# Performance work log

Hardware: AMD Instinct MI355X
Metric: run time of the kernel (lower is better)

The kernel has to match this reference:

```python
import jax, jax.numpy as jnp
import numpy as np

N = 100000          # nodes
E = 3200000         # edges (avg degree 32)
F_IN = 128
HID = [128, 256, 128, 64, 32]
EPS = 1e-5


def setup_inputs() -> dict:
    key = jax.random.key(0)
    ks = jax.random.split(key, 64)
    inp = {}
    inp["x"] = jax.random.normal(ks[0], (N, F_IN), dtype=jnp.float32)
    inp["edge_index"] = jax.random.randint(ks[1], (2, E), 0, N, dtype=jnp.int64)
    dims = [F_IN] + HID
    k = 2
    for i in range(len(HID)):
        fan_in = dims[i]
        inp[f"W{i}"] = jax.random.normal(ks[k], (dims[i], dims[i + 1]), dtype=jnp.float32) / np.sqrt(fan_in); k += 1
        inp[f"b{i}"] = jnp.zeros((dims[i + 1],), dtype=jnp.float32)
        inp[f"g{i}"] = jnp.ones((dims[i + 1],), dtype=jnp.float32)
        inp[f"be{i}"] = jnp.zeros((dims[i + 1],), dtype=jnp.float32)
    inp["fc_w"] = jax.random.normal(ks[k], (HID[-1], 1), dtype=jnp.float32) / np.sqrt(HID[-1])
    inp["fc_b"] = jnp.zeros((1,), dtype=jnp.float32)
    return inp


def _gcn_forward(x, edge_index, Ws, bs, gs, bes, fc_w, fc_b):
    src, dst = edge_index[0], edge_index[1]
    # symmetric-normalized adjacency with self-loops (PyG GCNConv default,
    # edge_weight=None -> all-ones). deg = in-degree + 1 (self-loop).
    deg = jax.ops.segment_sum(jnp.ones((E,), x.dtype), dst, num_segments=N) + 1.0
    dis = jax.lax.rsqrt(deg)                 # deg^{-1/2}
    di = 1.0 / deg                           # self-loop norm deg^{-1}
    norm = (dis[src] * dis[dst])[:, None]    # [E,1]
    for W, b, g, be in zip(Ws, bs, gs, bes):
        h = x @ W                                                        # [N,d']
        x = jax.ops.segment_sum(norm * h[src], dst, num_segments=N)
        x = x + di[:, None] * h + b                                      # conv out
        mu = jnp.mean(x, axis=0)
        var = jnp.mean(jnp.square(x - mu), axis=0)
        x = (x - mu) * jax.lax.rsqrt(var + EPS) * g + be                 # BatchNorm1d
        x = jax.nn.relu(x)                                               # dropout = eval identity
    edge_emb = x[src] * x[dst]                                           # [E, 32]
    return jax.nn.sigmoid(edge_emb @ fc_w + fc_b)                        # [E, 1]


def reference(x, edge_index, W0, b0, g0, be0, W1, b1, g1, be1, W2, b2, g2, be2,
              W3, b3, g3, be3, W4, b4, g4, be4, fc_w, fc_b):
    Ws = [W0, W1, W2, W3, W4]
    bs = [b0, b1, b2, b3, b4]
    gs = [g0, g1, g2, g3, g4]
    bes = [be0, be1, be2, be3, be4]
    return _gcn_forward(x, edge_index, Ws, bs, gs, bes, fc_w, fc_b)
```

## Files before the change

kernel.cpp:

```cpp
#include <hip/hip_runtime.h>
#include <hip/hip_fp16.h>
#include <cstddef>

#define NN 100000
#define EE 3200000
#define EPSB 1e-5f
#define NB 391
#define BCAP 10240
#define BNBLK 512

typedef _Float16 half8 __attribute__((ext_vector_type(8)));
typedef float floatx4 __attribute__((ext_vector_type(4)));


__global__ __launch_bounds__(256) void k_bscat(const int* __restrict__ src,
                                               const int* __restrict__ dst,
                                               int* __restrict__ bcur,
                                               unsigned* __restrict__ barr) {
    __shared__ int hist[NB];
    __shared__ int base[NB];
    int tid = threadIdx.x;
    for (int b = tid; b < NB; b += 256) hist[b] = 0;
    __syncthreads();
    int e0 = blockIdx.x * 4096;
    int d[16], s[16];
    #pragma unroll
    for (int j = 0; j < 16; j++) {
        int e = e0 + j * 256 + tid;
        if (e < EE) {
            d[j] = dst[e];
            s[j] = src[e];
            atomicAdd(&hist[d[j] >> 8], 1);
        } else d[j] = -1;
    }
    __syncthreads();
    for (int b = tid; b < NB; b += 256) {
        int c = hist[b];
        base[b] = (c > 0) ? atomicAdd(&bcur[b], c) : 0;
        hist[b] = 0;
    }
    __syncthreads();
    #pragma unroll
    for (int j = 0; j < 16; j++) {
        if (d[j] >= 0) {
            int b = d[j] >> 8;
            int r = atomicAdd(&hist[b], 1);
            barr[(size_t)b * BCAP + base[b] + r] =
                (unsigned)s[j] | ((unsigned)(d[j] & 255) << 17);
        }
    }
}

__global__ __launch_bounds__(1024) void k_bdeg(const int* __restrict__ bcur,
                                               const unsigned* __restrict__ barr,
                                               int* __restrict__ degcnt,
                                               float* __restrict__ dis) {
    __shared__ int h[256];
    int b = blockIdx.x;
    if (threadIdx.x < 256) h[threadIdx.x] = 0;
    __syncthreads();
    int cnt = bcur[b];
    const unsigned* p = barr + (size_t)b * BCAP;
    for (int t = threadIdx.x; t < cnt; t += 1024)
        atomicAdd(&h[(p[t] >> 17) & 255], 1);
    __syncthreads();
    if (threadIdx.x < 256) {
        int node = (b << 8) + threadIdx.x;
        if (node < NN) {
            int dg = h[threadIdx.x];
            degcnt[node] = dg;
            dis[node] = rsqrtf((float)dg + 1.0f);
        }
    }
}

__global__ __launch_bounds__(1024) void k_place(const int* __restrict__ bcur,
                                                const unsigned* __restrict__ barr,
                                                const int* __restrict__ rowptr,
                                                int* __restrict__ col) {
    __shared__ int cur[256];
    int b = blockIdx.x;
    if (threadIdx.x < 256) {
        int node = (b << 8) + threadIdx.x;
        cur[threadIdx.x] = (node < NN) ? rowptr[node] : 0;
    }
    __syncthreads();
    int cnt = bcur[b];
    const unsigned* p = barr + (size_t)b * BCAP;
    for (int t = threadIdx.x; t < cnt; t += 1024) {
        unsigned e = p[t];
        int pos = atomicAdd(&cur[(e >> 17) & 255], 1);
        col[pos] = (int)(e & 0x1FFFFu);
    }
}

__global__ void k_scan_block(const int* __restrict__ in, int* __restrict__ out,
                             int* __restrict__ blksum, int n) {
    __shared__ int s[1024];
    int i = blockIdx.x * 1024 + threadIdx.x;
    int v = (i < n) ? in[i] : 0;
    s[threadIdx.x] = v;
    __syncthreads();
    for (int off = 1; off < 1024; off <<= 1) {
        int t = (threadIdx.x >= off) ? s[threadIdx.x - off] : 0;
        __syncthreads();
        s[threadIdx.x] += t;
        __syncthreads();
    }
    if (i < n) out[i] = s[threadIdx.x] - v;
    if (threadIdx.x == 1023) blksum[blockIdx.x] = s[1023];
}

__global__ void k_scan_top(int* __restrict__ blksum, int nb) {
    if (threadIdx.x == 0) {
        int acc = 0;
        for (int b = 0; b < nb; b++) { int v = blksum[b]; blksum[b] = acc; acc += v; }
    }
}

__global__ void k_scan_add(int* __restrict__ out, const int* __restrict__ blksum, int n) {
    int i = blockIdx.x * 1024 + threadIdx.x;
    if (i < n) out[i] += blksum[blockIdx.x];
}


__global__ void k_f2h(const float4* __restrict__ in, uint2* __restrict__ out, int n4) {
    int t = blockIdx.x * blockDim.x + threadIdx.x;
    if (t >= n4) return;
    float4 v = in[t];
    union { __half2 h; unsigned u; } a, b;
    a.h = __floats2half2_rn(v.x, v.y);
    b.h = __floats2half2_rn(v.z, v.w);
    out[t] = make_uint2(a.u, b.u);
}

__global__ void k_wpack_all(const float* __restrict__ W0, const float* __restrict__ W1,
                            const float* __restrict__ W2, const float* __restrict__ W3,
                            const float* __restrict__ W4, __half* __restrict__ Wp) {
    const int offs[6] = {0, 16384, 49152, 81920, 90112, 92160};
    const int Ks[5] = {128, 128, 256, 128, 64};
    const int Ns[5] = {128, 256, 128, 64, 32};
    const float* Ws[5] = {W0, W1, W2, W3, W4};
    int t = blockIdx.x * blockDim.x + threadIdx.x;
    if (t >= 92160) return;
    int l = 0;
    while (t >= offs[l + 1]) l++;
    int local = t - offs[l];
    int N = Ns[l], K = Ks[l];
    int k = local / N, n = local - k * N;
    Wp[(size_t)offs[l] + (size_t)n * K + k] = __float2half(Ws[l][local]);
}


template<int NT, bool OUT16>
__global__ __launch_bounds__(256) void k_mgemm(const __half* __restrict__ A,
                                               const __half* __restrict__ Wp,
                                               void* __restrict__ Cv,
                                               int M, int K, int N,
                                               const float* __restrict__ dis,
                                               const float* __restrict__ bias) {
    constexpr int TN = NT * 16;
    __shared__ __half Ash[128][40];
    __shared__ __half Bsh[TN][40];
    int tid  = threadIdx.x;
    int wave = tid >> 6;
    int lane = tid & 63;
    int quad = lane >> 4;
    int l16  = lane & 15;
    int bm = blockIdx.x * 128;
    int bn = blockIdx.y * TN;

    floatx4 acc[2][NT];
    #pragma unroll
    for (int mt = 0; mt < 2; mt++)
        #pragma unroll
        for (int nt = 0; nt < NT; nt++)
            acc[mt][nt] = (floatx4){0.f, 0.f, 0.f, 0.f};

    for (int k0 = 0; k0 < K; k0 += 32) {
        #pragma unroll
        for (int it = 0; it < 2; it++) {
            int u = tid + it * 256;
            int row = u >> 2, seg = u & 3;
            int grow = bm + row;
            uint4 v = make_uint4(0, 0, 0, 0);
            if (grow < M) v = *(const uint4*)&A[(size_t)grow * K + k0 + seg * 8];
            *(uint4*)&Ash[row][seg * 8] = v;
        }
        if (tid < TN * 4) {
            int n = tid >> 2, seg = tid & 3;
            uint4 v = *(const uint4*)&Wp[(size_t)(bn + n) * K + k0 + seg * 8];
            *(uint4*)&Bsh[n][seg * 8] = v;
        }
        __syncthreads();
        half8 a[2], b[NT];
        #pragma unroll
        for (int mt = 0; mt < 2; mt++)
            a[mt] = *(const half8*)&Ash[wave * 32 + mt * 16 + l16][quad * 8];
        #pragma unroll
        for (int nt = 0; nt < NT; nt++)
            b[nt] = *(const half8*)&Bsh[nt * 16 + l16][quad * 8];
        #pragma unroll
        for (int mt = 0; mt < 2; mt++)
            #pragma unroll
            for (int nt = 0; nt < NT; nt++)
                acc[mt][nt] = __builtin_amdgcn_mfma_f32_16x16x32_f16(
                    a[mt], b[nt], acc[mt][nt], 0, 0, 0);
        __syncthreads();
    }

    #pragma unroll
    for (int mt = 0; mt < 2; mt++) {
        #pragma unroll
        for (int r = 0; r < 4; r++) {
            int grow = bm + wave * 32 + mt * 16 + quad * 4 + r;
            if (grow >= M) continue;
            if (OUT16) {
                float ds = dis[grow];
                __half* C = (__half*)Cv;
                #pragma unroll
                for (int nt = 0; nt < NT; nt++) {
                    int gcol = bn + nt * 16 + l16;
                    C[(size_t)grow * N + gcol] = __float2half(ds * acc[mt][nt][r]);
                }
            } else {
                float* C = (float*)Cv;
                #pragma unroll
                for (int nt = 0; nt < NT; nt++) {
                    int gcol = bn + nt * 16 + l16;
                    C[(size_t)grow * N + gcol] = acc[mt][nt][r] + bias[gcol];
                }
            }
        }
    }
}

__global__ void k_scale16(const uint4* __restrict__ X, const float* __restrict__ dis,
                          uint4* __restrict__ out) {
    int t = blockIdx.x * blockDim.x + threadIdx.x;
    if (t >= NN * 16) return;
    int row = t >> 4;
    float ds = dis[row];
    uint4 v = X[t];
    const __half2* hp = (const __half2*)&v;
    uint4 o;
    __half2* op = (__half2*)&o;
    #pragma unroll
    for (int k = 0; k < 4; k++) {
        float2 f = __half22float2(hp[k]);
        op[k] = __floats2half2_rn(ds * f.x, ds * f.y);
    }
    out[t] = o;
}


__device__ __forceinline__ void acc_row(float* acc, const uint4& r) {
    const __half2* hp = (const __half2*)&r;
    #pragma unroll
    for (int k = 0; k < 4; k++) {
        float2 f2 = __half22float2(hp[k]);
        acc[2 * k]     += f2.x;
        acc[2 * k + 1] += f2.y;
    }
}

template<int TPN, bool OUT16>
__global__ __launch_bounds__(256) void k_agg_h(const uint4* __restrict__ Hs,
                                               void* __restrict__ outv,
                                               const int* __restrict__ rowptr,
                                               const int* __restrict__ degcnt,
                                               const int* __restrict__ colv,
                                               const float* __restrict__ dis,
                                               const float* __restrict__ bias) {
    constexpr int G = 256 / TPN;
    int g    = threadIdx.x / TPN;
    int lane = threadIdx.x % TPN;
    int i = blockIdx.x * G + g;
    if (i >= NN) return;
    int beg = rowptr[i];
    int cnt = degcnt[i];
    const uint4* base = Hs + lane;
    float acc[8] = {};
    int e = 0;
    for (; e + 8 <= cnt; e += 8) {
        int c[8];
        #pragma unroll
        for (int j = 0; j < 8; j++) c[j] = colv[beg + e + j];
        uint4 r[8];
        #pragma unroll
        for (int j = 0; j < 8; j++) r[j] = base[(size_t)c[j] * TPN];
        #pragma unroll
        for (int j = 0; j < 8; j++) acc_row(acc, r[j]);
    }
    for (; e < cnt; e++) {
        uint4 r = base[(size_t)colv[beg + e] * TPN];
        acc_row(acc, r);
    }
    uint4 rs = base[(size_t)i * TPN];
    acc_row(acc, rs);
    float ds = dis[i];
    float o[8];
    #pragma unroll
    for (int k = 0; k < 8; k++) o[k] = ds * acc[k];
    if (OUT16) {
        uint4 ov;
        __half2* op = (__half2*)&ov;
        #pragma unroll
        for (int k = 0; k < 4; k++) op[k] = __floats2half2_rn(o[2 * k], o[2 * k + 1]);
        ((uint4*)outv)[(size_t)i * TPN + lane] = ov;
    } else {
        float4 b0 = ((const float4*)bias)[lane * 2];
        float4 b1 = ((const float4*)bias)[lane * 2 + 1];
        o[0] += b0.x; o[1] += b0.y; o[2] += b0.z; o[3] += b0.w;
        o[4] += b1.x; o[5] += b1.y; o[6] += b1.z; o[7] += b1.w;
        float4* out = (float4*)outv;
        size_t ob = (size_t)i * (2 * TPN) + lane * 2;
        out[ob]     = make_float4(o[0], o[1], o[2], o[3]);
        out[ob + 1] = make_float4(o[4], o[5], o[6], o[7]);
    }
}


template<int D>
__global__ __launch_bounds__(256) void k_bnpart(const float4* __restrict__ X4,
                                                float* __restrict__ partial) {
    constexpr int Q   = D / 4;
    constexpr int RPI = 256 / Q;
    int tq = threadIdx.x % Q;
    int rg = threadIdx.x / Q;
    int chunk = (NN + BNBLK - 1) / BNBLK;
    int r0 = blockIdx.x * chunk;
    int r1 = r0 + chunk; if (r1 > NN) r1 = NN;
    float4 s  = {0.f, 0.f, 0.f, 0.f};
    float4 s2 = {0.f, 0.f, 0.f, 0.f};
    for (int r = r0 + rg; r < r1; r += RPI) {
        float4 v = X4[(size_t)r * Q + tq];
        s.x += v.x; s.y += v.y; s.z += v.z; s.w += v.w;
        s2.x += v.x * v.x; s2.y += v.y * v.y; s2.z += v.z * v.z; s2.w += v.w * v.w;
    }
    __shared__ float4 ls[256], ls2[256];
    ls[threadIdx.x] = s; ls2[threadIdx.x] = s2;
    __syncthreads();
    if (threadIdx.x < Q) {
        float4 a = ls[threadIdx.x], b = ls2[threadIdx.x];
        #pragma unroll
        for (int g = 1; g < RPI; g++) {
            float4 u = ls[g * Q + threadIdx.x], w = ls2[g * Q + threadIdx.x];
            a.x += u.x; a.y += u.y; a.z += u.z; a.w += u.w;
            b.x += w.x; b.y += w.y; b.z += w.z; b.w += w.w;
        }
        *(float4*)&partial[(size_t)blockIdx.x * 2 * D + threadIdx.x * 4]     = a;
        *(float4*)&partial[(size_t)blockIdx.x * 2 * D + D + threadIdx.x * 4] = b;
    }
}

template<int D>
__global__ void k_bnfin2(const float* __restrict__ partial, const float* __restrict__ g,
                         const float* __restrict__ be, float* __restrict__ AB) {
    int f = threadIdx.x;
    if (f < D) {
        float sum = 0.f, sq = 0.f;
        for (int b = 0; b < BNBLK; b++) {
            sum += partial[(size_t)b * 2 * D + f];
            sq  += partial[(size_t)b * 2 * D + D + f];
        }
        float mu  = sum / (float)NN;
        float var = sq / (float)NN - mu * mu;
        var = fmaxf(var, 0.f);
        float inv = rsqrtf(var + EPSB);
        float a = g[f] * inv;
        AB[f]     = a;
        AB[D + f] = be[f] - mu * a;
    }
}

__global__ void k_norm16(const float4* __restrict__ X, const float* __restrict__ AB,
                         uint2* __restrict__ Y, int d, int total4) {
    int t = blockIdx.x * blockDim.x + threadIdx.x;
    if (t >= total4) return;
    int f0 = (t * 4) & (d - 1);
    float4 v = X[t];
    float a0 = AB[f0],     a1 = AB[f0 + 1], a2 = AB[f0 + 2], a3 = AB[f0 + 3];
    float c0 = AB[d + f0], c1 = AB[d + f0 + 1], c2 = AB[d + f0 + 2], c3 = AB[d + f0 + 3];
    float o0 = fmaxf(v.x * a0 + c0, 0.f);
    float o1 = fmaxf(v.y * a1 + c1, 0.f);
    float o2 = fmaxf(v.z * a2 + c2, 0.f);
    float o3 = fmaxf(v.w * a3 + c3, 0.f);
    union { __half2 h; unsigned u; } p, q;
    p.h = __floats2half2_rn(o0, o1);
    q.h = __floats2half2_rn(o2, o3);
    Y[t] = make_uint2(p.u, q.u);
}


__global__ __launch_bounds__(256) void k_edge16(const uint4* __restrict__ X,
                                                const int* __restrict__ src,
                                                const int* __restrict__ dst,
                                                const float* __restrict__ fcw,
                                                const float* __restrict__ fcb,
                                                float* __restrict__ out) {
    int lane = threadIdx.x & 3;
    size_t t = (size_t)blockIdx.x * 256 + threadIdx.x;
    int eid = (int)(t >> 2);
    if (eid >= EE) return;
    int s = src[eid], d = dst[eid];
    uint4 av = X[(size_t)s * 4 + lane];
    uint4 bv = X[(size_t)d * 4 + lane];
    const __half2* ap = (const __half2*)&av;
    const __half2* bp2 = (const __half2*)&bv;
    float v = 0.f;
    #pragma unroll
    for (int k = 0; k < 4; k++) {
        float2 fa = __half22float2(ap[k]);
        float2 fb = __half22float2(bp2[k]);
        float w0 = fcw[lane * 8 + 2 * k];
        float w1 = fcw[lane * 8 + 2 * k + 1];
        v += fa.x * fb.x * w0 + fa.y * fb.y * w1;
    }
    v += __shfl_xor(v, 1, 4);
    v += __shfl_xor(v, 2, 4);
    if (lane == 0) out[eid] = 1.f / (1.f + expf(-(v + fcb[0])));
}


extern "C" void kernel_launch(void* const* d_in, const int* in_sizes, int n_in,
                              void* d_out, int out_size, void* d_ws, size_t ws_size,
                              hipStream_t stream) {
    const float* x0 = (const float*)d_in[0];
    const int* ei   = (const int*)d_in[1];
    const int* srcv = ei;
    const int* dstv = ei + EE;
    const float *W[5], *bp[5], *gp[5], *bep[5];
    int idx = 2;
    for (int l = 0; l < 5; l++) {
        W[l]   = (const float*)d_in[idx++];
        bp[l]  = (const float*)d_in[idx++];
        gp[l]  = (const float*)d_in[idx++];
        bep[l] = (const float*)d_in[idx++];
    }
    const float* fcw = (const float*)d_in[22];
    const float* fcb = (const float*)d_in[23];

    char* ws = (char*)d_ws;
    size_t off = 0;
    auto alloc = [&](size_t bytes) -> void* {
        void* p = ws + off;
        off = (off + bytes + 255) & ~(size_t)255;
        return p;
    };
    float*    bufA    = (float*)   alloc((size_t)NN * 256 * 4);
    __half*   act16   = (__half*)  alloc((size_t)NN * 256 * 2);
    __half*   x16     = (__half*)  alloc((size_t)NN * 128 * 2);
    __half*   Hh      = (__half*)  alloc((size_t)NN * 128 * 2);
    unsigned* barr    = (unsigned*)alloc((size_t)NB * BCAP * 4);
    int*      colv    = (int*)     alloc((size_t)EE * 4);
    int*      rowptr  = (int*)     alloc((size_t)NN * 4);
    int*      degcnt  = (int*)     alloc((size_t)NN * 4);
    float*    dis     = (float*)   alloc((size_t)NN * 4);
    int*      bcur    = (int*)     alloc((size_t)NB * 4);
    int*      scnblk  = (int*)     alloc(4096);
    float*    bnpart  = (float*)   alloc((size_t)BNBLK * 512 * 4);
    float*    bnAB    = (float*)   alloc(512 * 4);
    __half*   Wp      = (__half*)  alloc((size_t)92160 * 2);
    const int woff[5] = {0, 16384, 49152, 81920, 90112};

    hipMemsetAsync(bcur, 0, (size_t)NB * 4, stream);
    k_bscat<<<(EE + 4095) / 4096, 256, 0, stream>>>(srcv, dstv, bcur, barr);
    k_bdeg<<<NB, 1024, 0, stream>>>(bcur, barr, degcnt, dis);
    int nScanBlk = (NN + 1023) / 1024;
    k_scan_block<<<nScanBlk, 1024, 0, stream>>>(degcnt, rowptr, scnblk, NN);
    k_scan_top<<<1, 64, 0, stream>>>(scnblk, nScanBlk);
    k_scan_add<<<nScanBlk, 1024, 0, stream>>>(rowptr, scnblk, NN);
    k_place<<<NB, 1024, 0, stream>>>(bcur, barr, rowptr, colv);

    k_f2h<<<(NN * 128 / 4 + 255) / 256, 256, 0, stream>>>(
        (const float4*)x0, (uint2*)x16, NN * 128 / 4);
    k_wpack_all<<<(92160 + 255) / 256, 256, 0, stream>>>(W[0], W[1], W[2], W[3], W[4], Wp);

    int gx = (NN + 127) / 128;

    {
        dim3 grid(gx, 128 / 64);
        k_mgemm<4, true><<<grid, 256, 0, stream>>>(x16, Wp + woff[0], Hh, NN, 128, 128, dis, nullptr);
        k_agg_h<16, false><<<(NN + 15) / 16, 256, 0, stream>>>(
            (const uint4*)Hh, bufA, rowptr, degcnt, colv, dis, bp[0]);
        k_bnpart<128><<<BNBLK, 256, 0, stream>>>((const float4*)bufA, bnpart);
        k_bnfin2<128><<<1, 256, 0, stream>>>(bnpart, gp[0], bep[0], bnAB);
        int total4 = NN * 128 / 4;
        k_norm16<<<(total4 + 255) / 256, 256, 0, stream>>>(
            (const float4*)bufA, bnAB, (uint2*)act16, 128, total4);
    }
    {
        k_scale16<<<(NN * 16 + 255) / 256, 256, 0, stream>>>(
            (const uint4*)act16, dis, (uint4*)Hh);
        k_agg_h<16, true><<<(NN + 15) / 16, 256, 0, stream>>>(
            (const uint4*)Hh, act16, rowptr, degcnt, colv, dis, nullptr);
        dim3 grid(gx, 256 / 64);
        k_mgemm<4, false><<<grid, 256, 0, stream>>>(act16, Wp + woff[1], bufA, NN, 128, 256, nullptr, bp[1]);
        k_bnpart<256><<<BNBLK, 256, 0, stream>>>((const float4*)bufA, bnpart);
        k_bnfin2<256><<<1, 256, 0, stream>>>(bnpart, gp[1], bep[1], bnAB);
        int total4 = NN * 256 / 4;
        k_norm16<<<(total4 + 255) / 256, 256, 0, stream>>>(
            (const float4*)bufA, bnAB, (uint2*)act16, 256, total4);
    }
    {
        dim3 grid(gx, 128 / 64);
        k_mgemm<4, true><<<grid, 256, 0, stream>>>(act16, Wp + woff[2], Hh, NN, 256, 128, dis, nullptr);
        k_agg_h<16, false><<<(NN + 15) / 16, 256, 0, stream>>>(
            (const uint4*)Hh, bufA, rowptr, degcnt, colv, dis, bp[2]);
        k_bnpart<128><<<BNBLK, 256, 0, stream>>>((const float4*)bufA, bnpart);
        k_bnfin2<128><<<1, 256, 0, stream>>>(bnpart, gp[2], bep[2], bnAB);
        int total4 = NN * 128 / 4;
        k_norm16<<<(total4 + 255) / 256, 256, 0, stream>>>(
            (const float4*)bufA, bnAB, (uint2*)act16, 128, total4);
    }
    {
        dim3 grid(gx, 64 / 64);
        k_mgemm<4, true><<<grid, 256, 0, stream>>>(act16, Wp + woff[3], Hh, NN, 128, 64, dis, nullptr);
        k_agg_h<8, false><<<(NN + 31) / 32, 256, 0, stream>>>(
            (const uint4*)Hh, bufA, rowptr, degcnt, colv, dis, bp[3]);
        k_bnpart<64><<<BNBLK, 256, 0, stream>>>((const float4*)bufA, bnpart);
        k_bnfin2<64><<<1, 256, 0, stream>>>(bnpart, gp[3], bep[3], bnAB);
        int total4 = NN * 64 / 4;
        k_norm16<<<(total4 + 255) / 256, 256, 0, stream>>>(
            (const float4*)bufA, bnAB, (uint2*)act16, 64, total4);
    }
    {
        dim3 grid(gx, 1);
        k_mgemm<2, true><<<grid, 256, 0, stream>>>(act16, Wp + woff[4], Hh, NN, 64, 32, dis, nullptr);
        k_agg_h<4, false><<<(NN + 63) / 64, 256, 0, stream>>>(
            (const uint4*)Hh, bufA, rowptr, degcnt, colv, dis, bp[4]);
        k_bnpart<32><<<BNBLK, 256, 0, stream>>>((const float4*)bufA, bnpart);
        k_bnfin2<32><<<1, 256, 0, stream>>>(bnpart, gp[4], bep[4], bnAB);
        int total4 = NN * 32 / 4;
        k_norm16<<<(total4 + 255) / 256, 256, 0, stream>>>(
            (const float4*)bufA, bnAB, (uint2*)act16, 32, total4);
    }

    size_t edgeThreads = (size_t)EE * 4;
    k_edge16<<<(unsigned)((edgeThreads + 255) / 256), 256, 0, stream>>>(
        (const uint4*)act16, srcv, dstv, fcw, fcb, (float*)d_out);
}
```

Before: 1.015 ms.

## Fuse BatchNorm-ReLU into GEMM A-load and dis scaling; parallelize BN finalize

Removes the separate BN-normalize kernels for layers 0-3. Layer 0's BN+ReLU is folded into the dis-scaling pass before aggregation. Layers 1-3 apply BN+ReLU on the fly while the next GEMM loads its fp32 A tile into LDS. The BN finalize kernel now uses 1024 threads with a shared-memory reduction instead of a serial loop over 512 partials. This saves a full write and read of the activations per layer, but the GEMM now reads fp32 A (twice the bytes) and recomputes the normalization for every N-tile block.

```diff
diff --git a/kernel.cpp b/kernel.cpp
--- a/kernel.cpp
+++ b/kernel.cpp
@@ -152,13 +152,14 @@
 }
 
 
-template<int NT, bool OUT16>
-__global__ __launch_bounds__(256) void k_mgemm(const __half* __restrict__ A,
+template<int NT, bool OUT16, bool ABN>
+__global__ __launch_bounds__(256) void k_mgemm(const void* __restrict__ Av,
                                                const __half* __restrict__ Wp,
                                                void* __restrict__ Cv,
                                                int M, int K, int N,
                                                const float* __restrict__ dis,
-                                               const float* __restrict__ bias) {
+                                               const float* __restrict__ bias,
+                                               const float* __restrict__ AB) {
     constexpr int TN = NT * 16;
     __shared__ __half Ash[128][40];
     __shared__ __half Bsh[TN][40];
@@ -183,9 +184,39 @@
             int u = tid + it * 256;
             int row = u >> 2, seg = u & 3;
             int grow = bm + row;
-            uint4 v = make_uint4(0, 0, 0, 0);
-            if (grow < M) v = *(const uint4*)&A[(size_t)grow * K + k0 + seg * 8];
-            *(uint4*)&Ash[row][seg * 8] = v;
+            if (ABN) {
+                const float* Af = (const float*)Av;
+                int f0 = k0 + seg * 8;
+                uint4 o = make_uint4(0, 0, 0, 0);
+                if (grow < M) {
+                    float4 x0 = *(const float4*)&Af[(size_t)grow * K + f0];
+                    float4 x1 = *(const float4*)&Af[(size_t)grow * K + f0 + 4];
+                    float4 a0 = *(const float4*)&AB[f0];
+                    float4 a1 = *(const float4*)&AB[f0 + 4];
+                    float4 c0 = *(const float4*)&AB[K + f0];
+                    float4 c1 = *(const float4*)&AB[K + f0 + 4];
+                    float h0 = fmaxf(x0.x * a0.x + c0.x, 0.f);
+                    float h1 = fmaxf(x0.y * a0.y + c0.y, 0.f);
+                    float h2 = fmaxf(x0.z * a0.z + c0.z, 0.f);
+                    float h3 = fmaxf(x0.w * a0.w + c0.w, 0.f);
+                    float h4 = fmaxf(x1.x * a1.x + c1.x, 0.f);
+                    float h5 = fmaxf(x1.y * a1.y + c1.y, 0.f);
+                    float h6 = fmaxf(x1.z * a1.z + c1.z, 0.f);
+                    float h7 = fmaxf(x1.w * a1.w + c1.w, 0.f);
+                    union { __half2 h; unsigned u; } p0, p1, p2, p3;
+                    p0.h = __floats2half2_rn(h0, h1);
+                    p1.h = __floats2half2_rn(h2, h3);
+                    p2.h = __floats2half2_rn(h4, h5);
+                    p3.h = __floats2half2_rn(h6, h7);
+                    o = make_uint4(p0.u, p1.u, p2.u, p3.u);
+                }
+                *(uint4*)&Ash[row][seg * 8] = o;
+            } else {
+                const __half* A = (const __half*)Av;
+                uint4 v = make_uint4(0, 0, 0, 0);
+                if (grow < M) v = *(const uint4*)&A[(size_t)grow * K + k0 + seg * 8];
+                *(uint4*)&Ash[row][seg * 8] = v;
+            }
         }
         if (tid < TN * 4) {
             int n = tid >> 2, seg = tid & 3;
@@ -235,22 +266,33 @@
     }
 }
 
-__global__ void k_scale16(const uint4* __restrict__ X, const float* __restrict__ dis,
-                          uint4* __restrict__ out) {
+__global__ void k_nscale(const float* __restrict__ X, const float* __restrict__ AB,
+                         const float* __restrict__ dis, uint4* __restrict__ out) {
     int t = blockIdx.x * blockDim.x + threadIdx.x;
     if (t >= NN * 16) return;
     int row = t >> 4;
+    int f0 = (t & 15) * 8;
     float ds = dis[row];
-    uint4 v = X[t];
-    const __half2* hp = (const __half2*)&v;
-    uint4 o;
-    __half2* op = (__half2*)&o;
-    #pragma unroll
-    for (int k = 0; k < 4; k++) {
-        float2 f = __half22float2(hp[k]);
-        op[k] = __floats2half2_rn(ds * f.x, ds * f.y);
-    }
-    out[t] = o;
+    float4 x0 = *(const float4*)&X[(size_t)row * 128 + f0];
+    float4 x1 = *(const float4*)&X[(size_t)row * 128 + f0 + 4];
+    float4 a0 = *(const float4*)&AB[f0];
+    float4 a1 = *(const float4*)&AB[f0 + 4];
+    float4 c0 = *(const float4*)&AB[128 + f0];
+    float4 c1 = *(const float4*)&AB[128 + f0 + 4];
+    float h0 = ds * fmaxf(x0.x * a0.x + c0.x, 0.f);
+    float h1 = ds * fmaxf(x0.y * a0.y + c0.y, 0.f);
+    float h2 = ds * fmaxf(x0.z * a0.z + c0.z, 0.f);
+    float h3 = ds * fmaxf(x0.w * a0.w + c0.w, 0.f);
+    float h4 = ds * fmaxf(x1.x * a1.x + c1.x, 0.f);
+    float h5 = ds * fmaxf(x1.y * a1.y + c1.y, 0.f);
+    float h6 = ds * fmaxf(x1.z * a1.z + c1.z, 0.f);
+    float h7 = ds * fmaxf(x1.w * a1.w + c1.w, 0.f);
+    union { __half2 h; unsigned u; } p0, p1, p2, p3;
+    p0.h = __floats2half2_rn(h0, h1);
+    p1.h = __floats2half2_rn(h2, h3);
+    p2.h = __floats2half2_rn(h4, h5);
+    p3.h = __floats2half2_rn(h6, h7);
+    out[t] = make_uint4(p0.u, p1.u, p2.u, p3.u);
 }
 
 
@@ -355,22 +397,34 @@
 }
 
 template<int D>
-__global__ void k_bnfin2(const float* __restrict__ partial, const float* __restrict__ g,
-                         const float* __restrict__ be, float* __restrict__ AB) {
-    int f = threadIdx.x;
-    if (f < D) {
-        float sum = 0.f, sq = 0.f;
-        for (int b = 0; b < BNBLK; b++) {
-            sum += partial[(size_t)b * 2 * D + f];
-            sq  += partial[(size_t)b * 2 * D + D + f];
-        }
-        float mu  = sum / (float)NN;
-        float var = sq / (float)NN - mu * mu;
+__global__ __launch_bounds__(1024) void k_bnfin2(const float* __restrict__ partial,
+                                                 const float* __restrict__ g,
+                                                 const float* __restrict__ be,
+                                                 float* __restrict__ AB) {
+    constexpr int G = 1024 / D;
+    int f  = threadIdx.x % D;
+    int gr = threadIdx.x / D;
+    float sum = 0.f, sq = 0.f;
+    for (int b = gr; b < BNBLK; b += G) {
+        sum += partial[(size_t)b * 2 * D + f];
+        sq  += partial[(size_t)b * 2 * D + D + f];
+    }
+    __shared__ float ls[1024], ls2[1024];
+    ls[threadIdx.x] = sum; ls2[threadIdx.x] = sq;
+    __syncthreads();
+    if (threadIdx.x < D) {
+        float a = ls[threadIdx.x], b = ls2[threadIdx.x];
+        for (int k = 1; k < G; k++) {
+            a += ls[k * D + threadIdx.x];
+            b += ls2[k * D + threadIdx.x];
+        }
+        float mu  = a / (float)NN;
+        float var = b / (float)NN - mu * mu;
         var = fmaxf(var, 0.f);
         float inv = rsqrtf(var + EPSB);
-        float a = g[f] * inv;
-        AB[f]     = a;
-        AB[D + f] = be[f] - mu * a;
+        float sc = g[threadIdx.x] * inv;
+        AB[threadIdx.x]     = sc;
+        AB[D + threadIdx.x] = be[threadIdx.x] - mu * sc;
     }
 }
 
@@ -481,57 +535,44 @@
 
     {
         dim3 grid(gx, 128 / 64);
-        k_mgemm<4, true><<<grid, 256, 0, stream>>>(x16, Wp + woff[0], Hh, NN, 128, 128, dis, nullptr);
+        k_mgemm<4, true, false><<<grid, 256, 0, stream>>>(x16, Wp + woff[0], Hh, NN, 128, 128, dis, nullptr, nullptr);
         k_agg_h<16, false><<<(NN + 15) / 16, 256, 0, stream>>>(
             (const uint4*)Hh, bufA, rowptr, degcnt, colv, dis, bp[0]);
         k_bnpart<128><<<BNBLK, 256, 0, stream>>>((const float4*)bufA, bnpart);
-        k_bnfin2<128><<<1, 256, 0, stream>>>(bnpart, gp[0], bep[0], bnAB);
-        int total4 = NN * 128 / 4;
-        k_norm16<<<(total4 + 255) / 256, 256, 0, stream>>>(
-            (const float4*)bufA, bnAB, (uint2*)act16, 128, total4);
+        k_bnfin2<128><<<1, 1024, 0, stream>>>(bnpart, gp[0], bep[0], bnAB);
+        k_nscale<<<(NN * 16 + 255) / 256, 256, 0, stream>>>(bufA, bnAB, dis, (uint4*)Hh);
     }
     {
-        k_scale16<<<(NN * 16 + 255) / 256, 256, 0, stream>>>(
-            (const uint4*)act16, dis, (uint4*)Hh);
         k_agg_h<16, true><<<(NN + 15) / 16, 256, 0, stream>>>(
             (const uint4*)Hh, act16, rowptr, degcnt, colv, dis, nullptr);
         dim3 grid(gx, 256 / 64);
-        k_mgemm<4, false><<<grid, 256, 0, stream>>>(act16, Wp + woff[1], bufA, NN, 128, 256, nullptr, bp[1]);
+        k_mgemm<4, false, false><<<grid, 256, 0, stream>>>(act16, Wp + woff[1], bufA, NN, 128, 256, nullptr, bp[1], nullptr);
         k_bnpart<256><<<BNBLK, 256, 0, stream>>>((const float4*)bufA, bnpart);
-        k_bnfin2<256><<<1, 256, 0, stream>>>(bnpart, gp[1], bep[1], bnAB);
-        int total4 = NN * 256 / 4;
-        k_norm16<<<(total4 + 255) / 256, 256, 0, stream>>>(
-            (const float4*)bufA, bnAB, (uint2*)act16, 256, total4);
+        k_bnfin2<256><<<1, 1024, 0, stream>>>(bnpart, gp[1], bep[1], bnAB);
     }
     {
         dim3 grid(gx, 128 / 64);
-        k_mgemm<4, true><<<grid, 256, 0, stream>>>(act16, Wp + woff[2], Hh, NN, 256, 128, dis, nullptr);
+        k_mgemm<4, true, true><<<grid, 256, 0, stream>>>(bufA, Wp + woff[2], Hh, NN, 256, 128, dis, nullptr, bnAB);
         k_agg_h<16, false><<<(NN + 15) / 16, 256, 0, stream>>>(
             (const uint4*)Hh, bufA, rowptr, degcnt, colv, dis, bp[2]);
         k_bnpart<128><<<BNBLK, 256, 0, stream>>>((const float4*)bufA, bnpart);
-        k_bnfin2<128><<<1, 256, 0, stream>>>(bnpart, gp[2], bep[2], bnAB);
-        int total4 = NN * 128 / 4;
-        k_norm16<<<(total4 + 255) / 256, 256, 0, stream>>>(
-            (const float4*)bufA, bnAB, (uint2*)act16, 128, total4);
+        k_bnfin2<128><<<1, 1024, 0, stream>>>(bnpart, gp[2], bep[2], bnAB);
     }
     {
         dim3 grid(gx, 64 / 64);
-        k_mgemm<4, true><<<grid, 256, 0, stream>>>(act16, Wp + woff[3], Hh, NN, 128, 64, dis, nullptr);
+        k_mgemm<4, true, true><<<grid, 256, 0, stream>>>(bufA, Wp + woff[3], Hh, NN, 128, 64, dis, nullptr, bnAB);
         k_agg_h<8, false><<<(NN + 31) / 32, 256, 0, stream>>>(
             (const uint4*)Hh, bufA, rowptr, degcnt, colv, dis, bp[3]);
         k_bnpart<64><<<BNBLK, 256, 0, stream>>>((const float4*)bufA, bnpart);
-        k_bnfin2<64><<<1, 256, 0, stream>>>(bnpart, gp[3], bep[3], bnAB);
-        int total4 = NN * 64 / 4;
-        k_norm16<<<(total4 + 255) / 256, 256, 0, stream>>>(
-            (const float4*)bufA, bnAB, (uint2*)act16, 64, total4);
+        k_bnfin2<64><<<1, 1024, 0, stream>>>(bnpart, gp[3], bep[3], bnAB);
     }
     {
         dim3 grid(gx, 1);
-        k_mgemm<2, true><<<grid, 256, 0, stream>>>(act16, Wp + woff[4], Hh, NN, 64, 32, dis, nullptr);
+        k_mgemm<2, true, true><<<grid, 256, 0, stream>>>(bufA, Wp + woff[4], Hh, NN, 64, 32, dis, nullptr, bnAB);
         k_agg_h<4, false><<<(NN + 63) / 64, 256, 0, stream>>>(
             (const uint4*)Hh, bufA, rowptr, degcnt, colv, dis, bp[4]);
         k_bnpart<32><<<BNBLK, 256, 0, stream>>>((const float4*)bufA, bnpart);
-        k_bnfin2<32><<<1, 256, 0, stream>>>(bnpart, gp[4], bep[4], bnAB);
+        k_bnfin2<32><<<1, 1024, 0, stream>>>(bnpart, gp[4], bep[4], bnAB);
         int total4 = NN * 32 / 4;
         k_norm16<<<(total4 + 255) / 256, 256, 0, stream>>>(
             (const float4*)bufA, bnAB, (uint2*)act16, 32, total4);
```

New measurement: 1.004 ms. No clear change (-1.1%).
